# Optimization experiments

Measured on AMD Instinct MI355X. Metric: run time of the kernel, lower is better.

The kernel has to match this reference:

```python
import jax, jax.numpy as jnp
import numpy as np

EPS = 1e-12  # tf.math.l2_normalize epsilon


def get_posenc(n, d):
    # Standard sinusoidal positional encoding, shape [n, d].
    pos = np.arange(n)[:, None].astype(np.float32)
    i = np.arange(d)[None, :]
    angle_rates = 1.0 / np.power(10000.0, (2 * (i // 2)).astype(np.float32) / np.float32(d))
    angles = pos * angle_rates
    pe = np.zeros((n, d), dtype=np.float32)
    pe[:, 0::2] = np.sin(angles[:, 0::2])
    pe[:, 1::2] = np.cos(angles[:, 1::2])
    return jnp.asarray(pe)


def setup_inputs() -> dict:
    key = jax.random.key(0)
    k1, k2, k3 = jax.random.split(key, 3)
    B, N, D = 4, 2048, 2048  # N must equal D (model_size) for the posenc matmul
    data = jax.random.normal(k1, (B, N, D), dtype=jnp.float32)
    W_exp = jax.random.normal(k2, (D + 1, D), dtype=jnp.float32) * (1.0 / np.sqrt(D + 1))
    b_exp = jnp.zeros((D,), dtype=jnp.float32)
    W_merge = jax.random.normal(k3, (2 * D, D), dtype=jnp.float32) * (1.0 / np.sqrt(2 * D))
    return {"data": data, "W_exp": W_exp, "b_exp": b_exp, "W_merge": W_merge}


def reference(data, W_exp, b_exp, W_merge):
    B, N, D = data.shape
    # l2 normalize along feature dim
    sq = jnp.sum(data * data, axis=-1, keepdims=True)
    cn = data * jax.lax.rsqrt(jnp.maximum(sq, EPS))
    # pairwise cosine similarity, rectified: [B, N, N]
    sim = jax.nn.relu(jnp.einsum("bnd,bmd->bnm", cn, cn))
    # fixed positional matmul: posenc [N, D] with D == N -> [B, N, N]
    fixed_v = get_posenc(N, D)
    v_output = jnp.einsum("nk,bkm->bnm", fixed_v, sim)
    # row-sum of similarities: [B, N, 1]
    csum = jnp.sum(sim, axis=-1, keepdims=True)
    counter = jnp.concatenate([csum, v_output], axis=-1)  # [B, N, N+1]
    counter = jax.nn.softplus(counter @ W_exp + b_exp)  # [B, N, D]
    out = jnp.concatenate([data, counter], axis=-1) @ W_merge  # [B, N, D]
    return out
```

## Files before the change

### kernel.cpp

```cpp
#include <hip/hip_runtime.h>

#define B_ 4
#define N_ 2048
#define D_ 2048

#define BM 128
#define BN 128
#define BK 32
#define TP 136

typedef __bf16 bf16x8 __attribute__((ext_vector_type(8)));
typedef float  f32x4  __attribute__((ext_vector_type(4)));

__device__ __forceinline__ ushort f2bf(float x) {
  union { float f; unsigned u; } c; c.f = x;
  unsigned u = c.u;
  u += 0x7fffu + ((u >> 16) & 1u);
  return (ushort)(u >> 16);
}

__device__ __forceinline__ void gld16(ushort* lds, const ushort* g) {
  __builtin_amdgcn_global_load_lds(
      (const __attribute__((address_space(1))) void*)g,
      (__attribute__((address_space(3))) void*)lds, 16, 0, 0);
}


__global__ void prep_cn(const float* __restrict__ data, ushort* __restrict__ cn,
                        ushort* __restrict__ catA) {
  const int row = blockIdx.x;
  const long base = (long)row * D_;
  const float4* r4 = (const float4*)(data + base);
  const int tid = threadIdx.x;
  float4 u0 = r4[tid * 2], u1 = r4[tid * 2 + 1];
  float s = u0.x*u0.x + u0.y*u0.y + u0.z*u0.z + u0.w*u0.w
          + u1.x*u1.x + u1.y*u1.y + u1.z*u1.z + u1.w*u1.w;
  #pragma unroll
  for (int o = 32; o > 0; o >>= 1) s += __shfl_down(s, o);
  __shared__ float wsum[4];
  if ((tid & 63) == 0) wsum[tid >> 6] = s;
  __syncthreads();
  const float tot = wsum[0] + wsum[1] + wsum[2] + wsum[3];
  const float sc = rsqrtf(fmaxf(tot, 1e-12f));
  uint4 pc, pd;
  pc.x = (unsigned)f2bf(u0.x * sc) | ((unsigned)f2bf(u0.y * sc) << 16);
  pc.y = (unsigned)f2bf(u0.z * sc) | ((unsigned)f2bf(u0.w * sc) << 16);
  pc.z = (unsigned)f2bf(u1.x * sc) | ((unsigned)f2bf(u1.y * sc) << 16);
  pc.w = (unsigned)f2bf(u1.z * sc) | ((unsigned)f2bf(u1.w * sc) << 16);
  pd.x = (unsigned)f2bf(u0.x) | ((unsigned)f2bf(u0.y) << 16);
  pd.y = (unsigned)f2bf(u0.z) | ((unsigned)f2bf(u0.w) << 16);
  pd.z = (unsigned)f2bf(u1.x) | ((unsigned)f2bf(u1.y) << 16);
  pd.w = (unsigned)f2bf(u1.z) | ((unsigned)f2bf(u1.w) << 16);
  *(uint4*)(cn + base + tid * 8) = pc;
  *(uint4*)(catA + (long)row * (2 * D_) + tid * 8) = pd;
}

__global__ void prep_pe(ushort* __restrict__ pe) {
  const int id = blockIdx.x * 256 + threadIdx.x;
  const int n = id >> 11, d = id & (D_ - 1);
  const float e = (float)(2 * (d >> 1)) * (1.0f / (float)D_);
  const float rate = expf(e * -9.210340371976184f);
  const float ang = (float)n * rate;
  const float v = (d & 1) ? cosf(ang) : sinf(ang);
  pe[id] = f2bf(v);
}

__global__ void transpose_bf16(const float* __restrict__ in, ushort* __restrict__ out,
                               int R, int C) {
  __shared__ float t[32][33];
  const int c0 = blockIdx.x * 32, r0 = blockIdx.y * 32;
  const int tx = threadIdx.x, ty = threadIdx.y;
  #pragma unroll
  for (int i = 0; i < 32; i += 8) t[ty + i][tx] = in[(long)(r0 + ty + i) * C + c0 + tx];
  __syncthreads();
  #pragma unroll
  for (int i = 0; i < 32; i += 8) out[(long)(c0 + ty + i) * R + r0 + tx] = f2bf(t[tx][ty + i]);
}

__global__ __launch_bounds__(256, 2) void gemm_sym(
    const ushort* __restrict__ Ag, ushort* __restrict__ Cg, float* __restrict__ csum) {
  __shared__ ushort sAt[BM * BK];
  __shared__ ushort sBt[BN * BK];
  __shared__ ushort tile[128 * TP];

  const int bz = blockIdx.z;
  const int t = blockIdx.x;
  int bj = (int)((sqrtf(8.f * (float)t + 1.f) - 1.f) * 0.5f);
  while ((bj + 1) * (bj + 2) / 2 <= t) bj++;
  while (bj * (bj + 1) / 2 > t) bj--;
  const int bi = t - bj * (bj + 1) / 2;

  const ushort* A = Ag + (long)bz * N_ * D_;
  const int blockRow = bi * BM;
  const int blockCol = bj * BN;

  const int tid = threadIdx.x;
  const int w = tid >> 6, L = tid & 63;
  const int ldRow = w * 16 + (L >> 2);
  const int ldK = (((L & 3) ^ ((L >> 3) & 3)) * 8);
  const ushort* a0 = A + (long)(blockRow + ldRow) * D_ + ldK;
  const ushort* a1 = a0 + (long)64 * D_;
  const ushort* b0 = A + (long)(blockCol + ldRow) * D_ + ldK;
  const ushort* b1 = b0 + (long)64 * D_;
  ushort* sA0 = sAt + w * 512;
  ushort* sA1 = sAt + 2048 + w * 512;
  ushort* sB0 = sBt + w * 512;
  ushort* sB1 = sBt + 2048 + w * 512;

  const int wm = (w & 1) * 64, wn = (w >> 1) * 64;
  const int fr = L & 15;
  const int sw = (((L >> 4) ^ ((fr >> 1) & 3)) * 8);

  f32x4 acc[4][4] = {};
  for (int k0 = 0; k0 < D_; k0 += BK) {
    gld16(sA0, a0); gld16(sA1, a1);
    gld16(sB0, b0); gld16(sB1, b1);
    a0 += BK; a1 += BK; b0 += BK; b1 += BK;
    __syncthreads();
    bf16x8 af[4], bfv[4];
    #pragma unroll
    for (int i = 0; i < 4; i++) af[i]  = *(const bf16x8*)&sAt[(wm + i * 16 + fr) * BK + sw];
    #pragma unroll
    for (int j = 0; j < 4; j++) bfv[j] = *(const bf16x8*)&sBt[(wn + j * 16 + fr) * BK + sw];
    #pragma unroll
    for (int i = 0; i < 4; i++)
      #pragma unroll
      for (int j = 0; j < 4; j++)
        acc[i][j] = __builtin_amdgcn_mfma_f32_16x16x32_bf16(af[i], bfv[j], acc[i][j], 0, 0, 0);
    __syncthreads();
  }

  const int rq = (L >> 4) * 4;
  const int cq = L & 15;
  ushort* C = Cg + (long)bz * N_ * N_;

  float rs[4][4];
  float cs[4];
  #pragma unroll
  for (int i = 0; i < 4; i++)
    #pragma unroll
    for (int r = 0; r < 4; r++) rs[i][r] = 0.f;
  #pragma unroll
  for (int j = 0; j < 4; j++) cs[j] = 0.f;

  const bool offdiag = (bi != bj);

  #pragma unroll
  for (int i = 0; i < 4; i++)
    #pragma unroll
    for (int j = 0; j < 4; j++)
      #pragma unroll
      for (int r = 0; r < 4; r++) {
        const float v = fmaxf(acc[i][j][r], 0.f);
        rs[i][r] += v;
        cs[j] += v;
        tile[(wm + i * 16 + rq + r) * TP + wn + j * 16 + cq] = f2bf(v);
      }
  __syncthreads();
  {
    const int rp = tid >> 1, h = tid & 1;
    const ushort* src = &tile[rp * TP + h * 64];
    ushort* dst = &C[(long)(blockRow + rp) * N_ + blockCol + h * 64];
    #pragma unroll
    for (int q = 0; q < 8; q++)
      *(uint4*)(dst + q * 8) = *(const uint4*)(src + q * 8);
  }

  #pragma unroll
  for (int i = 0; i < 4; i++)
    #pragma unroll
    for (int r = 0; r < 4; r++) {
      float s = rs[i][r];
      s += __shfl_xor(s, 1); s += __shfl_xor(s, 2);
      s += __shfl_xor(s, 4); s += __shfl_xor(s, 8);
      if (cq == 0)
        atomicAdd(&csum[(long)bz * N_ + blockRow + wm + i * 16 + rq + r], s);
    }

  if (offdiag) {
    #pragma unroll
    for (int j = 0; j < 4; j++) {
      float s = cs[j];
      s += __shfl_xor(s, 16); s += __shfl_xor(s, 32);
      if (L < 16)
        atomicAdd(&csum[(long)bz * N_ + blockCol + wn + j * 16 + cq], s);
    }
    __syncthreads();
    #pragma unroll
    for (int i = 0; i < 4; i++)
      #pragma unroll
      for (int j = 0; j < 4; j++)
        #pragma unroll
        for (int r = 0; r < 4; r++) {
          const float v = fmaxf(acc[i][j][r], 0.f);
          tile[(wn + j * 16 + cq) * TP + wm + i * 16 + rq + r] = f2bf(v);
        }
    __syncthreads();
    const int rp = tid >> 1, h = tid & 1;
    const ushort* src = &tile[rp * TP + h * 64];
    ushort* dst = &C[(long)(blockCol + rp) * N_ + blockRow + h * 64];
    #pragma unroll
    for (int q = 0; q < 8; q++)
      *(uint4*)(dst + q * 8) = *(const uint4*)(src + q * 8);
  }
}


__device__ __forceinline__ void stage_half(ushort* d, const ushort* s, int K) {
  gld16(d, s);
  gld16(d + 4096, s + (long)64 * K);
}

template <int M0>
__device__ __forceinline__ void rd_a(const ushort* __restrict__ T, int aO0, int aO1,
                                     bf16x8 (&af)[2][2]) {
  af[0][0] = *(const bf16x8*)&T[aO0 + M0 * 1024];
  af[0][1] = *(const bf16x8*)&T[aO1 + M0 * 1024];
  af[1][0] = *(const bf16x8*)&T[aO0 + (M0 + 1) * 1024];
  af[1][1] = *(const bf16x8*)&T[aO1 + (M0 + 1) * 1024];
}

__device__ __forceinline__ void rd_b8(const ushort* __restrict__ T, int bO0, int bO1,
                                      bf16x8 (&bf)[4][2]) {
  #pragma unroll
  for (int j = 0; j < 4; j++) {
    bf[j][0] = *(const bf16x8*)&T[bO0 + j * 1024];
    bf[j][1] = *(const bf16x8*)&T[bO1 + j * 1024];
  }
}

template <int M0>
__device__ __forceinline__ void mfma16(const bf16x8 (&af)[2][2], const bf16x8 (&bf)[4][2],
                                       f32x4 (&acc)[8][4]) {
  #pragma unroll
  for (int kk = 0; kk < 2; kk++)
    #pragma unroll
    for (int mm = 0; mm < 2; mm++)
      #pragma unroll
      for (int j = 0; j < 4; j++)
        acc[M0 + mm][j] = __builtin_amdgcn_mfma_f32_16x16x32_bf16(
            af[mm][kk], bf[j][kk], acc[M0 + mm][j], 0, 0, 0);
}

#define W_LGKM0 asm volatile("s_waitcnt lgkmcnt(0)" ::: "memory")
#define W_VM4   asm volatile("s_waitcnt vmcnt(4)" ::: "memory")
#define W_VM0   asm volatile("s_waitcnt vmcnt(0)" ::: "memory")
#define SBAR    asm volatile("s_barrier" ::: "memory")
#define SCHB    __builtin_amdgcn_sched_barrier(0)
#define PRIO1   __builtin_amdgcn_s_setprio(1)
#define PRIO0   __builtin_amdgcn_s_setprio(0)

template <int MODE>
__global__ __launch_bounds__(512, 2) void gemm8(
    const ushort* __restrict__ Ag, const ushort* __restrict__ Bg, void* __restrict__ Cg,
    int K, long sA, long sB, long sC, int ldc, int colOff,
    const float* __restrict__ csum, const float* __restrict__ w0,
    const float* __restrict__ bexp) {
  extern __shared__ ushort lds[];

  const int lin = blockIdx.x + (blockIdx.y << 3) + (blockIdx.z << 6);
  const int xcd = lin & 7, m_ = lin >> 3;
  const int bz = xcd >> 1;
  const int by = ((xcd & 1) << 2) + (m_ >> 3);
  const int bx = m_ & 7;

  const ushort* A  = Ag + (long)bz * sA + (long)(bx << 8) * K;
  const ushort* Bp = Bg + (long)bz * sB + (long)(by << 8) * K;

  const int tid = threadIdx.x;
  const int sr = tid >> 3;
  const int sc = ((tid & 7) ^ (sr & 7)) << 3;
  const ushort* aS = A + (long)sr * K + sc;
  const ushort* bS = Bp + (long)sr * K + sc;
  const int wOff = (tid >> 6) << 9;
  ushort* const stA0 = lds + wOff;
  ushort* const stA1 = lds + 16384 + wOff;
  ushort* const stB0 = lds + 32768 + wOff;
  ushort* const stB1 = lds + 49152 + wOff;
  const ushort* const TA0 = lds;          const ushort* const TA1 = lds + 16384;
  const ushort* const TB0 = lds + 32768;  const ushort* const TB1 = lds + 49152;

  auto stg = [&](ushort* base, const ushort* src, int T, int H) {
    stage_half(base + (H << 13), src + (long)(H << 7) * K + ((long)T << 6), K);
  };

  const int L = tid & 63, wid = tid >> 6;
  const int wr = wid >> 2, wc = wid & 3;
  const int fr = L & 15, g = L >> 4;
  const int off0 = ((g ^ (fr & 7)) << 3);
  const int aO0 = ((wr << 7) + fr) * 64 + off0, aO1 = aO0 ^ 32;
  const int bO0 = ((wc << 6) + fr) * 64 + off0, bO1 = bO0 ^ 32;

  f32x4 acc[8][4] = {};
  bf16x8 af[2][2], bf[4][2];

  const int NT = K >> 6, NTI = NT >> 1;

  stg(stB0, bS, 0, 0); stg(stB0, bS, 0, 1); stg(stA0, aS, 0, 0); stg(stA0, aS, 0, 1);
  stg(stB1, bS, 1, 0); stg(stB1, bS, 1, 1);
  stg(stA1, aS, 1, 0);
  asm volatile("s_waitcnt vmcnt(6)" ::: "memory");
  SBAR;
  rd_b8(TB0, bO0, bO1, bf);
  rd_a<0>(TA0, aO0, aO1, af);

  for (int it = 0; it < NTI; ++it) {
    const int t1 = 2 * it + 1, t2 = 2 * it + 2, t3 = 2 * it + 3;
    const bool more = (it + 1 < NTI);

    stg(stA1, aS, t1, 1);
    W_LGKM0; SCHB;
    PRIO1; mfma16<0>(af, bf, acc); PRIO0; SCHB;
    rd_a<2>(TA0, aO0, aO1, af);
    SBAR;
    if (more) stg(stB0, bS, t2, 0);
    W_LGKM0; SCHB;
    PRIO1; mfma16<2>(af, bf, acc); PRIO0; SCHB;
    rd_a<4>(TA0, aO0, aO1, af);
    SBAR;
    if (more) stg(stB0, bS, t2, 1);
    W_LGKM0; SCHB;
    PRIO1; mfma16<4>(af, bf, acc); PRIO0; SCHB;
    rd_a<6>(TA0, aO0, aO1, af);
    SBAR;
    W_LGKM0;
    if (more) { W_VM4; } else { W_VM0; }
    SBAR;
    SCHB;
    PRIO1; mfma16<6>(af, bf, acc); PRIO0; SCHB;
    rd_b8(TB1, bO0, bO1, bf);
    rd_a<0>(TA1, aO0, aO1, af);
    SBAR;
    if (more) stg(stA0, aS, t2, 0);
    W_LGKM0; SCHB;
    PRIO1; mfma16<0>(af, bf, acc); PRIO0; SCHB;
    rd_a<2>(TA1, aO0, aO1, af);
    SBAR;
    if (more) stg(stA0, aS, t2, 1);
    W_LGKM0; SCHB;
    PRIO1; mfma16<2>(af, bf, acc); PRIO0; SCHB;
    rd_a<4>(TA1, aO0, aO1, af);
    SBAR;
    if (more) stg(stB1, bS, t3, 0);
    W_LGKM0; SCHB;
    PRIO1; mfma16<4>(af, bf, acc); PRIO0; SCHB;
    rd_a<6>(TA1, aO0, aO1, af);
    SBAR;
    if (more) stg(stB1, bS, t3, 1);
    W_LGKM0;
    if (more) { W_VM4; }
    SBAR;
    SCHB;
    PRIO1; mfma16<6>(af, bf, acc); PRIO0; SCHB;
    if (more) {
      rd_b8(TB0, bO0, bO1, bf);
      rd_a<0>(TA0, aO0, aO1, af);
      stg(stA1, aS, t3, 0);
    }
    SBAR;
  }

  const int cq = fr;
  const int rowB0 = (bx << 8) + (wr << 7);
  const int colB0 = (by << 8) + (wc << 6);

  if (MODE == 3) {
    float* eT = (float*)lds + (size_t)wid * 1088;
    float* Cb = (float*)Cg + (long)bz * sC;
    const int er = L >> 4, ec = L & 15;
    #pragma unroll
    for (int m = 0; m < 8; m++) {
      #pragma unroll
      for (int j = 0; j < 4; j++)
        #pragma unroll
        for (int r = 0; r < 4; r++)
          eT[(g * 4 + r) * 68 + j * 16 + cq] = acc[m][j][r];
      #pragma unroll
      for (int q = 0; q < 4; q++) {
        const f32x4 v = *(const f32x4*)&eT[(er + q * 4) * 68 + ec * 4];
        const long row = rowB0 + m * 16 + er + q * 4;
        *(f32x4*)&Cb[row * ldc + colB0 + ec * 4] = v;
      }
    }
  } else {
    ushort* eT = lds + (size_t)wid * 1152;
    ushort* Cb = (ushort*)Cg + (long)bz * sC;
    const int er = L >> 3, ec = L & 7;
    float w0v[4], bev[4];
    if (MODE == 2) {
      #pragma unroll
      for (int j = 0; j < 4; j++) {
        w0v[j] = w0[colB0 + j * 16 + cq];
        bev[j] = bexp[colB0 + j * 16 + cq];
      }
    }
    #pragma unroll
    for (int m = 0; m < 8; m++) {
      #pragma unroll
      for (int j = 0; j < 4; j++)
        #pragma unroll
        for (int r = 0; r < 4; r++) {
          float x = acc[m][j][r];
          if (MODE == 2) {
            const float cv = csum[(long)bz * N_ + rowB0 + m * 16 + g * 4 + r];
            x = x + cv * w0v[j] + bev[j];
            x = fmaxf(x, 0.f) + log1pf(expf(-fabsf(x)));
          }
          eT[(g * 4 + r) * 72 + j * 16 + cq] = f2bf(x);
        }
      #pragma unroll
      for (int q = 0; q < 2; q++) {
        const uint4 v = *(const uint4*)&eT[(er + q * 8) * 72 + ec * 8];
        const long row = rowB0 + m * 16 + er + q * 8;
        *(uint4*)&Cb[row * ldc + colOff + colB0 + ec * 8] = v;
      }
    }
  }
}

extern "C" void kernel_launch(void* const* d_in, const int* in_sizes, int n_in,
                              void* d_out, int out_size, void* d_ws, size_t ws_size,
                              hipStream_t stream) {
  const float* data    = (const float*)d_in[0];
  const float* W_exp   = (const float*)d_in[1];
  const float* b_exp   = (const float*)d_in[2];
  const float* W_merge = (const float*)d_in[3];

  char* ws = (char*)d_ws;
  const size_t MB = 1024 * 1024;
  ushort* cnv  = (ushort*)(ws);
  ushort* sim  = (ushort*)(ws + 32 * MB);
  ushort* pe   = (ushort*)(ws + 64 * MB);
  ushort* weT  = (ushort*)(ws + 72 * MB);
  ushort* wmT  = (ushort*)(ws + 80 * MB);
  ushort* catA = (ushort*)(ws + 96 * MB);
  float*  csum = (float*)(ws + 160 * MB);

  static bool attrs_set = false;
  if (!attrs_set) {
    (void)hipFuncSetAttribute((const void*)gemm8<1>, hipFuncAttributeMaxDynamicSharedMemorySize, 131072);
    (void)hipFuncSetAttribute((const void*)gemm8<2>, hipFuncAttributeMaxDynamicSharedMemorySize, 131072);
    (void)hipFuncSetAttribute((const void*)gemm8<3>, hipFuncAttributeMaxDynamicSharedMemorySize, 131072);
    attrs_set = true;
  }

  hipMemsetAsync(csum, 0, (size_t)B_ * N_ * sizeof(float), stream);
  prep_cn<<<B_ * N_, 256, 0, stream>>>(data, cnv, catA);
  prep_pe<<<(N_ * N_) / 256, 256, 0, stream>>>(pe);
  transpose_bf16<<<dim3(D_ / 32, D_ / 32), dim3(32, 8), 0, stream>>>(W_exp + D_, weT, D_, D_);
  transpose_bf16<<<dim3(D_ / 32, (2 * D_) / 32), dim3(32, 8), 0, stream>>>(W_merge, wmT, 2 * D_, D_);

  gemm_sym<<<dim3(136, 1, B_), dim3(256), 0, stream>>>(cnv, sim, csum);

  dim3 g8(N_ / 256, N_ / 256, B_);
  gemm8<1><<<g8, 512, 131072, stream>>>(pe, sim, cnv, N_, 0, (long)N_ * N_,
                                        (long)N_ * N_, N_, 0, nullptr, nullptr, nullptr);
  gemm8<2><<<g8, 512, 131072, stream>>>(cnv, weT, catA, N_, (long)N_ * N_, 0,
                                        (long)N_ * 2 * D_, 2 * D_, D_, csum, W_exp, b_exp);
  gemm8<3><<<g8, 512, 131072, stream>>>(catA, wmT, d_out, 2 * D_, (long)N_ * 2 * D_, 0,
                                        (long)N_ * D_, D_, 0, nullptr, nullptr, nullptr);
}
```

Before: 500.2 us.

## Replace symmetric similarity GEMM with full tuned gemm8 kernel plus fused row-sum

Removes the triangular symmetric gemm_sym kernel (128x128 tiles, 256 threads, simple sync loop) and computes the full cn·cnᵀ similarity matrix with the pipelined 256x256 gemm8 kernel in a new MODE 4. That mode applies ReLU and accumulates row sums with atomics. This roughly doubles the FLOPs for the similarity product but uses the more efficient, better-pipelined kernel and drops the transposed mirror writes and the column-sum atomics. Correctness relies on gemm8's bf16 epilogue path handling MODE 4 like the other bf16 modes.

```diff
diff --git a/kernel.cpp b/kernel.cpp
--- a/kernel.cpp
+++ b/kernel.cpp
@@ -3,11 +3,6 @@
 #define B_ 4
 #define N_ 2048
 #define D_ 2048
-
-#define BM 128
-#define BN 128
-#define BK 32
-#define TP 136
 
 typedef __bf16 bf16x8 __attribute__((ext_vector_type(8)));
 typedef float  f32x4  __attribute__((ext_vector_type(4)));
@@ -77,134 +72,6 @@
   for (int i = 0; i < 32; i += 8) out[(long)(c0 + ty + i) * R + r0 + tx] = f2bf(t[tx][ty + i]);
 }
 
-__global__ __launch_bounds__(256, 2) void gemm_sym(
-    const ushort* __restrict__ Ag, ushort* __restrict__ Cg, float* __restrict__ csum) {
-  __shared__ ushort sAt[BM * BK];
-  __shared__ ushort sBt[BN * BK];
-  __shared__ ushort tile[128 * TP];
-
-  const int bz = blockIdx.z;
-  const int t = blockIdx.x;
-  int bj = (int)((sqrtf(8.f * (float)t + 1.f) - 1.f) * 0.5f);
-  while ((bj + 1) * (bj + 2) / 2 <= t) bj++;
-  while (bj * (bj + 1) / 2 > t) bj--;
-  const int bi = t - bj * (bj + 1) / 2;
-
-  const ushort* A = Ag + (long)bz * N_ * D_;
-  const int blockRow = bi * BM;
-  const int blockCol = bj * BN;
-
-  const int tid = threadIdx.x;
-  const int w = tid >> 6, L = tid & 63;
-  const int ldRow = w * 16 + (L >> 2);
-  const int ldK = (((L & 3) ^ ((L >> 3) & 3)) * 8);
-  const ushort* a0 = A + (long)(blockRow + ldRow) * D_ + ldK;
-  const ushort* a1 = a0 + (long)64 * D_;
-  const ushort* b0 = A + (long)(blockCol + ldRow) * D_ + ldK;
-  const ushort* b1 = b0 + (long)64 * D_;
-  ushort* sA0 = sAt + w * 512;
-  ushort* sA1 = sAt + 2048 + w * 512;
-  ushort* sB0 = sBt + w * 512;
-  ushort* sB1 = sBt + 2048 + w * 512;
-
-  const int wm = (w & 1) * 64, wn = (w >> 1) * 64;
-  const int fr = L & 15;
-  const int sw = (((L >> 4) ^ ((fr >> 1) & 3)) * 8);
-
-  f32x4 acc[4][4] = {};
-  for (int k0 = 0; k0 < D_; k0 += BK) {
-    gld16(sA0, a0); gld16(sA1, a1);
-    gld16(sB0, b0); gld16(sB1, b1);
-    a0 += BK; a1 += BK; b0 += BK; b1 += BK;
-    __syncthreads();
-    bf16x8 af[4], bfv[4];
-    #pragma unroll
-    for (int i = 0; i < 4; i++) af[i]  = *(const bf16x8*)&sAt[(wm + i * 16 + fr) * BK + sw];
-    #pragma unroll
-    for (int j = 0; j < 4; j++) bfv[j] = *(const bf16x8*)&sBt[(wn + j * 16 + fr) * BK + sw];
-    #pragma unroll
-    for (int i = 0; i < 4; i++)
-      #pragma unroll
-      for (int j = 0; j < 4; j++)
-        acc[i][j] = __builtin_amdgcn_mfma_f32_16x16x32_bf16(af[i], bfv[j], acc[i][j], 0, 0, 0);
-    __syncthreads();
-  }
-
-  const int rq = (L >> 4) * 4;
-  const int cq = L & 15;
-  ushort* C = Cg + (long)bz * N_ * N_;
-
-  float rs[4][4];
-  float cs[4];
-  #pragma unroll
-  for (int i = 0; i < 4; i++)
-    #pragma unroll
-    for (int r = 0; r < 4; r++) rs[i][r] = 0.f;
-  #pragma unroll
-  for (int j = 0; j < 4; j++) cs[j] = 0.f;
-
-  const bool offdiag = (bi != bj);
-
-  #pragma unroll
-  for (int i = 0; i < 4; i++)
-    #pragma unroll
-    for (int j = 0; j < 4; j++)
-      #pragma unroll
-      for (int r = 0; r < 4; r++) {
-        const float v = fmaxf(acc[i][j][r], 0.f);
-        rs[i][r] += v;
-        cs[j] += v;
-        tile[(wm + i * 16 + rq + r) * TP + wn + j * 16 + cq] = f2bf(v);
-      }
-  __syncthreads();
-  {
-    const int rp = tid >> 1, h = tid & 1;
-    const ushort* src = &tile[rp * TP + h * 64];
-    ushort* dst = &C[(long)(blockRow + rp) * N_ + blockCol + h * 64];
-    #pragma unroll
-    for (int q = 0; q < 8; q++)
-      *(uint4*)(dst + q * 8) = *(const uint4*)(src + q * 8);
-  }
-
-  #pragma unroll
-  for (int i = 0; i < 4; i++)
-    #pragma unroll
-    for (int r = 0; r < 4; r++) {
-      float s = rs[i][r];
-      s += __shfl_xor(s, 1); s += __shfl_xor(s, 2);
-      s += __shfl_xor(s, 4); s += __shfl_xor(s, 8);
-      if (cq == 0)
-        atomicAdd(&csum[(long)bz * N_ + blockRow + wm + i * 16 + rq + r], s);
-    }
-
-  if (offdiag) {
-    #pragma unroll
-    for (int j = 0; j < 4; j++) {
-      float s = cs[j];
-      s += __shfl_xor(s, 16); s += __shfl_xor(s, 32);
-      if (L < 16)
-        atomicAdd(&csum[(long)bz * N_ + blockCol + wn + j * 16 + cq], s);
-    }
-    __syncthreads();
-    #pragma unroll
-    for (int i = 0; i < 4; i++)
-      #pragma unroll
-      for (int j = 0; j < 4; j++)
-        #pragma unroll
-        for (int r = 0; r < 4; r++) {
-          const float v = fmaxf(acc[i][j][r], 0.f);
-          tile[(wn + j * 16 + cq) * TP + wm + i * 16 + rq + r] = f2bf(v);
-        }
-    __syncthreads();
-    const int rp = tid >> 1, h = tid & 1;
-    const ushort* src = &tile[rp * TP + h * 64];
-    ushort* dst = &C[(long)(blockCol + rp) * N_ + blockRow + h * 64];
-    #pragma unroll
-    for (int q = 0; q < 8; q++)
-      *(uint4*)(dst + q * 8) = *(const uint4*)(src + q * 8);
-  }
-}
-
 
 __device__ __forceinline__ void stage_half(ushort* d, const ushort* s, int K) {
   gld16(d, s);
@@ -254,7 +121,7 @@
 __global__ __launch_bounds__(512, 2) void gemm8(
     const ushort* __restrict__ Ag, const ushort* __restrict__ Bg, void* __restrict__ Cg,
     int K, long sA, long sB, long sC, int ldc, int colOff,
-    const float* __restrict__ csum, const float* __restrict__ w0,
+    float* __restrict__ csum, const float* __restrict__ w0,
     const float* __restrict__ bexp) {
   extern __shared__ ushort lds[];
 
@@ -396,6 +263,7 @@
     }
     #pragma unroll
     for (int m = 0; m < 8; m++) {
+      float rsr[4] = {0.f, 0.f, 0.f, 0.f};
       #pragma unroll
       for (int j = 0; j < 4; j++)
         #pragma unroll
@@ -406,8 +274,22 @@
             x = x + cv * w0v[j] + bev[j];
             x = fmaxf(x, 0.f) + log1pf(expf(-fabsf(x)));
           }
+          if (MODE == 4) {
+            x = fmaxf(x, 0.f);
+            rsr[r] += x;
+          }
           eT[(g * 4 + r) * 72 + j * 16 + cq] = f2bf(x);
         }
+      if (MODE == 4) {
+        #pragma unroll
+        for (int r = 0; r < 4; r++) {
+          float s = rsr[r];
+          s += __shfl_xor(s, 1); s += __shfl_xor(s, 2);
+          s += __shfl_xor(s, 4); s += __shfl_xor(s, 8);
+          if (fr == 0)
+            atomicAdd(&csum[(long)bz * N_ + rowB0 + m * 16 + g * 4 + r], s);
+        }
+      }
       #pragma unroll
       for (int q = 0; q < 2; q++) {
         const uint4 v = *(const uint4*)&eT[(er + q * 8) * 72 + ec * 8];
@@ -441,6 +323,7 @@
     (void)hipFuncSetAttribute((const void*)gemm8<1>, hipFuncAttributeMaxDynamicSharedMemorySize, 131072);
     (void)hipFuncSetAttribute((const void*)gemm8<2>, hipFuncAttributeMaxDynamicSharedMemorySize, 131072);
     (void)hipFuncSetAttribute((const void*)gemm8<3>, hipFuncAttributeMaxDynamicSharedMemorySize, 131072);
+    (void)hipFuncSetAttribute((const void*)gemm8<4>, hipFuncAttributeMaxDynamicSharedMemorySize, 131072);
     attrs_set = true;
   }
 
@@ -450,9 +333,9 @@
   transpose_bf16<<<dim3(D_ / 32, D_ / 32), dim3(32, 8), 0, stream>>>(W_exp + D_, weT, D_, D_);
   transpose_bf16<<<dim3(D_ / 32, (2 * D_) / 32), dim3(32, 8), 0, stream>>>(W_merge, wmT, 2 * D_, D_);
 
-  gemm_sym<<<dim3(136, 1, B_), dim3(256), 0, stream>>>(cnv, sim, csum);
-
   dim3 g8(N_ / 256, N_ / 256, B_);
+  gemm8<4><<<g8, 512, 131072, stream>>>(cnv, cnv, sim, N_, (long)N_ * D_, (long)N_ * D_,
+                                        (long)N_ * N_, N_, 0, csum, nullptr, nullptr);
   gemm8<1><<<g8, 512, 131072, stream>>>(pe, sim, cnv, N_, 0, (long)N_ * N_,
                                         (long)N_ * N_, N_, 0, nullptr, nullptr, nullptr);
   gemm8<2><<<g8, 512, 131072, stream>>>(cnv, weT, catA, N_, (long)N_ * N_, 0,
```

Result: no change. 490.7 us (-1.9%).
